# Kernel optimization log

Measured on AMD Instinct MI355X. Metric: run time of the kernel, lower is better.

## Reference

```python
import jax, jax.numpy as jnp
import numpy as np

B, N = 64, 1024
DIMS = [1, 32, 64, 64, 1]   # dim after insert(0,1) and append(1)
DEGS = [2, 2, 2, 2]
EPS = 1e-5


def setup_inputs() -> dict:
    key = jax.random.key(0)
    ks = jax.random.split(key, 16)
    inp = {
        "e": jax.random.uniform(ks[0], (B, N), jnp.float32),
        "phi": jax.random.normal(ks[1], (B, N), jnp.float32),
        "eta": jax.random.normal(ks[2], (B, N), jnp.float32),
    }
    for i in range(4):
        fan_in = DIMS[i] * DEGS[i]
        inp[f"W{i}"] = jax.random.normal(ks[3 + 2 * i], (DIMS[i + 1], fan_in), jnp.float32) / np.sqrt(fan_in)
        inp[f"b{i}"] = jnp.zeros((DIMS[i + 1],), jnp.float32)
    return inp


def _gconv(adj, x, W, b, deg):
    # x: [B, C, N], adj: [B, N, N]
    # operators: [x, x@A, x@A^2, ...] up to deg powers (A^0 = identity)
    ops = [x]
    for _ in range(deg - 1):
        ops.append(jnp.einsum('bcn,bnm->bcm', ops[-1], adj))
    cat = jnp.concatenate(ops, axis=1)                 # [B, C*deg, N]
    return jnp.einsum('oc,bcn->bon', W, cat) + b[None, :, None]


def reference(e, phi, eta, W0, b0, W1, b1, W2, b2, W3, b3):
    # batchnorm(e, axis=1): standardize each event over its particles
    mu = e.mean(axis=1, keepdims=True)
    sd = e.std(axis=1, keepdims=True)
    e = (e - mu) / (sd + EPS)
    e = e[:, None, :]                                   # [B, 1, N]

    # Adjacency: gaussian kernel of squared euclidean distance in (phi, eta)
    d2 = (phi[:, :, None] - phi[:, None, :]) ** 2 + (eta[:, :, None] - eta[:, None, :]) ** 2
    adj = jnp.exp(-d2)                                  # [B, N, N]

    Ws = (W0, W1, W2, W3)
    bs = (b0, b1, b2, b3)
    for i in range(3):
        e = jax.nn.relu(_gconv(adj, e, Ws[i], bs[i], DEGS[i]))
    e = _gconv(adj, e, Ws[3], bs[3], DEGS[3])           # [B, 1, N]

    out = e.mean(axis=2)[:, 0]                          # [B], + logistic_bias (=0)
    return jax.nn.sigmoid(out)
```

## Files before the change

### kernel.cpp

```cpp
#include <hip/hip_runtime.h>
#include <hip/hip_bf16.h>
#include <math.h>

#define BB 64
#define NN 1024
#define EPSV 1e-5f

typedef unsigned short u16;
typedef __attribute__((ext_vector_type(8))) short short8;
typedef __attribute__((ext_vector_type(4))) float f32x4;

#define GLOBAL_AS __attribute__((address_space(1)))
#define LDS_AS __attribute__((address_space(3)))

#define SCL 1.20112240878645f

static __device__ __forceinline__ void gload_lds16(const void* g, void* l) {
  __builtin_amdgcn_global_load_lds((const GLOBAL_AS unsigned int*)g,
                                   (LDS_AS unsigned int*)l, 16, 0, 0);
}

static __device__ __forceinline__ u16 f2bf(float f) {
  __hip_bfloat16 h = __float2bfloat16(f);
  union { __hip_bfloat16 h; u16 s; } u; u.h = h; return u.s;
}
static __device__ __forceinline__ float bf2f(u16 s) {
  unsigned int u = ((unsigned int)s) << 16;
  union { unsigned int u; float f; } c; c.u = u; return c.f;
}
static __device__ __forceinline__ float expn2(float dp, float de) {
#if __has_builtin(__builtin_amdgcn_exp2f)
  return __builtin_amdgcn_exp2f(fmaf(-dp, dp, -(de * de)));
#else
  return exp2f(fmaf(-dp, dp, -(de * de)));
#endif
}

__global__ __launch_bounds__(256, 4) void fused0_kernel(
    const float* __restrict__ e,
    const float* __restrict__ phi, const float* __restrict__ eta,
    const float* __restrict__ W0, const float* __restrict__ b0,
    const float* __restrict__ W1, const float* __restrict__ W2,
    u16* __restrict__ Wp1, u16* __restrict__ Wp2,
    u16* __restrict__ ZN,
    u16* __restrict__ ZC)
{
  __shared__ float x0[NN];
  __shared__ float2 pe[NN];
  __shared__ float red[256];
  __shared__ u16 zt[64 * 40];

  int b = blockIdx.y;
  int m0 = blockIdx.x * 64;
  int tid = threadIdx.x;

  if (blockIdx.x == 0 && b == 0)
    for (int i = tid; i < 64 * 64; i += 256) Wp1[i] = f2bf(W1[i]);
  if (blockIdx.x == 0 && b == 1)
    for (int i = tid; i < 64 * 128; i += 256) Wp2[i] = f2bf(W2[i]);

  const float* er = e + (size_t)b * NN;
  const float* phb = phi + (size_t)b * NN;
  const float* etb = eta + (size_t)b * NN;

  float s = 0.f;
  for (int i = tid; i < NN; i += 256) {
    float v = er[i]; x0[i] = v; s += v;
    pe[i] = make_float2(phb[i] * SCL, etb[i] * SCL);
  }
  red[tid] = s; __syncthreads();
  for (int off = 128; off > 0; off >>= 1) {
    if (tid < off) red[tid] += red[tid + off];
    __syncthreads();
  }
  float mu = red[0] * (1.f / NN);
  __syncthreads();
  float s2 = 0.f;
  for (int i = tid; i < NN; i += 256) { float d = x0[i] - mu; s2 += d * d; }
  red[tid] = s2; __syncthreads();
  for (int off = 128; off > 0; off >>= 1) {
    if (tid < off) red[tid] += red[tid + off];
    __syncthreads();
  }
  float sd = sqrtf(red[0] * (1.f / NN));
  float inv = 1.f / (sd + EPSV);
  for (int i = tid; i < NN; i += 256) x0[i] = (x0[i] - mu) * inv;
  __syncthreads();

  int q = tid >> 6;
  int mi = tid & 63;
  int m = m0 + mi;
  float phm = pe[m].x, etm = pe[m].y;

  const float2* pp = &pe[q * 256];
  const float* xx = &x0[q * 256];
  float t0a = 0.f, t0b = 0.f;
#pragma unroll 4
  for (int n = 0; n < 256; n += 2) {
    float2 qa = pp[n], qb = pp[n + 1];
    float dpa = qa.x - phm, dea = qa.y - etm;
    float dpb = qb.x - phm, deb = qb.y - etm;
    t0a = fmaf(expn2(dpa, dea), xx[n], t0a);
    t0b = fmaf(expn2(dpb, deb), xx[n + 1], t0b);
  }
  red[q * 64 + mi] = t0a + t0b;
  __syncthreads();
  float t0 = (red[0 * 64 + mi] + red[1 * 64 + mi]) +
             (red[2 * 64 + mi] + red[3 * 64 + mi]);

  float x0m = x0[m];
  union { short8 v; u16 h[8]; } zrow;
#pragma unroll
  for (int oj = 0; oj < 8; ++oj) {
    int o = q * 8 + oj;
    float z = fmaf(W0[o * 2], x0m, fmaf(W0[o * 2 + 1], t0, b0[o]));
    zrow.h[oj] = f2bf(fmaxf(z, 0.f));
  }
  *(short8*)&ZN[((size_t)b * NN + m) * 32 + q * 8] = zrow.v;
  *(short8*)&zt[mi * 40 + q * 8] = zrow.v;
  __syncthreads();
  for (int idx = tid; idx < 64 * 32; idx += 256) {
    int mm = idx & 63, o = idx >> 6;
    ZC[((size_t)b * 32 + o) * NN + m0 + mm] = zt[mm * 40 + o];
  }
}

template<int CE, int O, int NT>
__global__ __launch_bounds__(256, 4) void fused_kernel(
    const u16* __restrict__ XC,
    const u16* __restrict__ XN,
    const float* __restrict__ phi,
    const float* __restrict__ eta,
    const u16* __restrict__ Wp,
    const float* __restrict__ bias,
    u16* __restrict__ ZN,
    u16* __restrict__ ZC)
{
  constexpr int NCT = CE / 16;
  constexpr int SLABV = NT * CE / 8;
  constexpr int KW = 2 * CE;
  constexpr int S = KW + 8;
  constexpr int OT = O / 16;
  constexpr int KS = KW / 32;
  constexpr int STEPS = NN / NT;
  constexpr int KCN = NT / 32;

  constexpr int PH1 = (int)sizeof(float2) * NN + 2 * NT * CE * 2;
  constexpr int PH2 = 64 * S * 2;
  constexpr int ZTS = 64 * (O + 8) * 2;
  constexpr int SM0 = PH1 > PH2 ? PH1 : PH2;
  constexpr int SM = SM0 > ZTS ? SM0 : ZTS;
  __shared__ __align__(16) char smem[SM];
  float2* pe = (float2*)smem;
  u16* slab0 = (u16*)(smem + sizeof(float2) * NN);
  u16* slab1 = slab0 + NT * CE;
  u16* cat = (u16*)smem;
  u16* zt  = (u16*)smem;

  int b = blockIdx.y;
  int m0 = blockIdx.x * 64;
  int tid = threadIdx.x;
  int lane = tid & 63, w = tid >> 6, g = lane >> 4, cl = lane & 15;

  const float* phb = phi + (size_t)b * NN;
  const float* etb = eta + (size_t)b * NN;
  for (int i = tid; i < NN; i += 256)
    pe[i] = make_float2(phb[i] * SCL, etb[i] * SCL);

  int m_lane = m0 + w * 16 + cl;
  float phm = phb[m_lane] * SCL;
  float etm = etb[m_lane] * SCL;

  f32x4 acc[NCT];
#pragma unroll
  for (int ci = 0; ci < NCT; ++ci) acc[ci] = (f32x4){0.f, 0.f, 0.f, 0.f};

  const u16* xb = XC + (size_t)b * CE * NN;

  for (int v = tid; v < SLABV; v += 256) {
    int gg = v / CE, cc = (v % CE) ^ (gg & 7);
    gload_lds16(xb + (size_t)cc * NN + gg * 8, slab0 + v * 8);
  }
  __syncthreads();

  for (int s = 0; s < STEPS; ++s) {
    u16* curp = (s & 1) ? slab1 : slab0;
    u16* nxtp = (s & 1) ? slab0 : slab1;
    if (s + 1 < STEPS) {
      for (int v = tid; v < SLABV; v += 256) {
        int gg = v / CE, cc = (v % CE) ^ (gg & 7);
        gload_lds16(xb + (size_t)cc * NN + (s + 1) * NT + gg * 8, nxtp + v * 8);
      }
    }
    int n0 = s * NT;
#pragma unroll
    for (int kc = 0; kc < KCN; ++kc) {
      const float2* pp = &pe[n0 + kc * 32 + 8 * g];
      union { short8 v; u16 h[8]; } af;
#pragma unroll
      for (int j = 0; j < 8; ++j) {
        float2 qq = pp[j];
        af.h[j] = f2bf(expn2(qq.x - phm, qq.y - etm));
      }
      int ggr = kc * 4 + g, sw = ggr & 7;
#pragma unroll
      for (int ci = 0; ci < NCT; ++ci) {
        const short8* bp =
            (const short8*)&curp[(ggr * CE + ((ci * 16 + cl) ^ sw)) * 8];
        acc[ci] = __builtin_amdgcn_mfma_f32_16x16x32_bf16(af.v, *bp, acc[ci], 0, 0, 0);
      }
    }
    __syncthreads();
  }

  constexpr int CV = CE / 8;
  constexpr int NXN = (64 * CV + 255) / 256;
  constexpr bool XFULL = (64 * CV) % 256 == 0;
  short8 xnr[NXN];
#pragma unroll
  for (int i = 0; i < NXN; ++i) {
    int v = tid + i * 256;
    if (XFULL || v < 64 * CV) {
      int m = v / CV, cv = v % CV;
      xnr[i] = *(const short8*)&XN[((size_t)b * NN + m0 + m) * CE + cv * 8];
    }
  }
  float bz[OT];
#pragma unroll
  for (int oi = 0; oi < OT; ++oi) bz[oi] = bias[oi * 16 + cl];

#pragma unroll
  for (int ci = 0; ci < NCT; ++ci)
#pragma unroll
    for (int r = 0; r < 4; ++r) {
      int m = w * 16 + g * 4 + r;
      cat[m * S + CE + ci * 16 + cl] = f2bf(acc[ci][r]);
    }
#pragma unroll
  for (int i = 0; i < NXN; ++i) {
    int v = tid + i * 256;
    if (XFULL || v < 64 * CV) {
      int m = v / CV, cv = v % CV;
      *(short8*)&cat[m * S + cv * 8] = xnr[i];
    }
  }
  __syncthreads();

  short8 afp[KS];
#pragma unroll
  for (int kk = 0; kk < KS; ++kk)
    afp[kk] = *(const short8*)&cat[(w * 16 + cl) * S + kk * 32 + g * 8];

  constexpr int OB = (8 / KS) < OT ? (8 / KS) : OT;
  f32x4 pacc[OT];
#pragma unroll
  for (int oi = 0; oi < OT; ++oi) pacc[oi] = (f32x4){0.f, 0.f, 0.f, 0.f};
#pragma unroll
  for (int ob = 0; ob < OT; ob += OB) {
    short8 wfr[OB][KS];
#pragma unroll
    for (int oi = 0; oi < OB; ++oi)
#pragma unroll
      for (int kk = 0; kk < KS; ++kk)
        wfr[oi][kk] = *(const short8*)&Wp[((ob + oi) * 16 + cl) * KW + kk * 32 + g * 8];
#pragma unroll
    for (int oi = 0; oi < OB; ++oi)
#pragma unroll
      for (int kk = 0; kk < KS; ++kk)
        pacc[ob + oi] = __builtin_amdgcn_mfma_f32_16x16x32_bf16(
            afp[kk], wfr[oi][kk], pacc[ob + oi], 0, 0, 0);
  }
  __syncthreads();

#pragma unroll
  for (int oi = 0; oi < OT; ++oi) {
#pragma unroll
    for (int r = 0; r < 4; ++r) {
      float z = fmaxf(pacc[oi][r] + bz[oi], 0.f);
      u16 zb = f2bf(z);
      int m = w * 16 + 4 * g + r;
      ZN[((size_t)b * NN + m0 + m) * O + oi * 16 + cl] = zb;
      zt[m * (O + 8) + oi * 16 + cl] = zb;
    }
  }
  __syncthreads();
  for (int idx = tid; idx < 64 * O; idx += 256) {
    int m = idx & 63, o = idx >> 6;
    ZC[((size_t)b * O + o) * NN + m0 + m] = zt[m * (O + 8) + o];
  }
}

__global__ __launch_bounds__(256, 4) void fused_last_kernel(
    const u16* __restrict__ XC,
    const u16* __restrict__ XN,
    const float* __restrict__ phi,
    const float* __restrict__ eta,
    const float* __restrict__ W3,
    const float* __restrict__ b3,
    float* __restrict__ partial)
{
  constexpr int CE = 64, NCT = 4, NT = 128;
  constexpr int SLABV = NT * CE / 8;
  constexpr int S = 136;
  constexpr int STEPS = NN / NT;

  constexpr int PH1 = (int)sizeof(float2) * NN + 2 * NT * CE * 2;
  __shared__ __align__(16) char smem[PH1];
  float2* pe = (float2*)smem;
  u16* slab0 = (u16*)(smem + sizeof(float2) * NN);
  u16* slab1 = slab0 + NT * CE;
  u16* cat = (u16*)smem;
  float* sW = (float*)(smem + 17408);
  float* red = (float*)(smem + 17408 + 512);

  int b = blockIdx.y;
  int m0 = blockIdx.x * 64;
  int tid = threadIdx.x;
  int lane = tid & 63, w = tid >> 6, g = lane >> 4, cl = lane & 15;

  const float* phb = phi + (size_t)b * NN;
  const float* etb = eta + (size_t)b * NN;
  for (int i = tid; i < NN; i += 256)
    pe[i] = make_float2(phb[i] * SCL, etb[i] * SCL);

  int m_lane = m0 + w * 16 + cl;
  float phm = phb[m_lane] * SCL;
  float etm = etb[m_lane] * SCL;

  f32x4 acc[NCT];
#pragma unroll
  for (int ci = 0; ci < NCT; ++ci) acc[ci] = (f32x4){0.f, 0.f, 0.f, 0.f};

  const u16* xb = XC + (size_t)b * CE * NN;

  for (int v = tid; v < SLABV; v += 256) {
    int gg = v / CE, cc = (v % CE) ^ (gg & 7);
    gload_lds16(xb + (size_t)cc * NN + gg * 8, slab0 + v * 8);
  }
  __syncthreads();

  for (int s = 0; s < STEPS; ++s) {
    u16* curp = (s & 1) ? slab1 : slab0;
    u16* nxtp = (s & 1) ? slab0 : slab1;
    if (s + 1 < STEPS) {
      for (int v = tid; v < SLABV; v += 256) {
        int gg = v / CE, cc = (v % CE) ^ (gg & 7);
        gload_lds16(xb + (size_t)cc * NN + (s + 1) * NT + gg * 8, nxtp + v * 8);
      }
    }
    int n0 = s * NT;
#pragma unroll
    for (int kc = 0; kc < NT / 32; ++kc) {
      const float2* pp = &pe[n0 + kc * 32 + 8 * g];
      union { short8 v; u16 h[8]; } af;
#pragma unroll
      for (int j = 0; j < 8; ++j) {
        float2 qq = pp[j];
        af.h[j] = f2bf(expn2(qq.x - phm, qq.y - etm));
      }
      int ggr = kc * 4 + g, sw = ggr & 7;
#pragma unroll
      for (int ci = 0; ci < NCT; ++ci) {
        const short8* bp =
            (const short8*)&curp[(ggr * CE + ((ci * 16 + cl) ^ sw)) * 8];
        acc[ci] = __builtin_amdgcn_mfma_f32_16x16x32_bf16(af.v, *bp, acc[ci], 0, 0, 0);
      }
    }
    __syncthreads();
  }

  short8 xnr0, xnr1;
  {
    int v0 = tid, v1 = tid + 256;
    int ma = v0 >> 3, ca = v0 & 7, mb = v1 >> 3, cb = v1 & 7;
    xnr0 = *(const short8*)&XN[((size_t)b * NN + m0 + ma) * CE + ca * 8];
    xnr1 = *(const short8*)&XN[((size_t)b * NN + m0 + mb) * CE + cb * 8];
  }
  if (tid < 128) sW[tid] = W3[tid];
#pragma unroll
  for (int ci = 0; ci < NCT; ++ci)
#pragma unroll
    for (int r = 0; r < 4; ++r) {
      int m = w * 16 + g * 4 + r;
      cat[m * S + CE + ci * 16 + cl] = f2bf(acc[ci][r]);
    }
  {
    int v0 = tid, v1 = tid + 256;
    int ma = v0 >> 3, ca = v0 & 7, mb = v1 >> 3, cb = v1 & 7;
    *(short8*)&cat[ma * S + ca * 8] = xnr0;
    *(short8*)&cat[mb * S + cb * 8] = xnr1;
  }
  __syncthreads();

  int m = tid & 63, q = tid >> 6;
  float sacc = 0.f;
#pragma unroll
  for (int v = 0; v < 4; ++v) {
    short8 cv = *(const short8*)&cat[m * S + q * 32 + v * 8];
#pragma unroll
    for (int j = 0; j < 8; ++j)
      sacc = fmaf(sW[q * 32 + v * 8 + j], bf2f((u16)cv[j]), sacc);
  }
  red[tid] = sacc; __syncthreads();
  for (int off = 128; off > 0; off >>= 1) {
    if (tid < off) red[tid] += red[tid + off];
    __syncthreads();
  }
  if (tid == 0)
    partial[b * 16 + blockIdx.x] = red[0] + 64.f * b3[0];
}

__global__ __launch_bounds__(64) void final_kernel(const float* __restrict__ partial,
                                                   float* __restrict__ out) {
  int b = blockIdx.x;
  int lane = threadIdx.x;
  float v = (lane < 16) ? partial[b * 16 + lane] : 0.f;
#pragma unroll
  for (int off = 8; off > 0; off >>= 1) v += __shfl_down(v, off);
  if (lane == 0) out[b] = 1.f / (1.f + __expf(-(v * (1.f / NN))));
}

extern "C" void kernel_launch(void* const* d_in, const int* in_sizes, int n_in,
                              void* d_out, int out_size, void* d_ws, size_t ws_size,
                              hipStream_t stream) {
  const float* e   = (const float*)d_in[0];
  const float* phi = (const float*)d_in[1];
  const float* eta = (const float*)d_in[2];
  const float* W0  = (const float*)d_in[3];
  const float* b0  = (const float*)d_in[4];
  const float* W1  = (const float*)d_in[5];
  const float* b1  = (const float*)d_in[6];
  const float* W2  = (const float*)d_in[7];
  const float* b2  = (const float*)d_in[8];
  const float* W3  = (const float*)d_in[9];
  const float* b3  = (const float*)d_in[10];

  char* wsb = (char*)d_ws;
  const size_t MB = 1u << 20;
  float* PB = (float*)(wsb);
  u16* XC1 = (u16*)(wsb + 12 * MB);
  u16* XN1 = (u16*)(wsb + 16 * MB);
  u16* XC2 = (u16*)(wsb + 20 * MB);
  u16* XN2 = (u16*)(wsb + 28 * MB);
  u16* XC3 = (u16*)(wsb + 8 * MB);
  u16* XN3 = (u16*)(wsb + 36 * MB);
  u16* Wp1 = (u16*)(wsb + 44 * MB);
  u16* Wp2 = Wp1 + 64 * 64;

  dim3 blk(256);
  dim3 gg(NN / 64, BB);

  fused0_kernel<<<gg, blk, 0, stream>>>(e, phi, eta, W0, b0, W1, W2,
                                        Wp1, Wp2, XN1, XC1);
  fused_kernel<32, 64, 128><<<gg, blk, 0, stream>>>(XC1, XN1, phi, eta, Wp1, b1, XN2, XC2);
  fused_kernel<64, 64, 128><<<gg, blk, 0, stream>>>(XC2, XN2, phi, eta, Wp2, b2, XN3, XC3);
  fused_last_kernel<<<gg, blk, 0, stream>>>(XC3, XN3, phi, eta, W3, b3, PB);

  final_kernel<<<BB, dim3(64), 0, stream>>>(PB, (float*)d_out);
}
```

Measured before the change: 113.1 us.

## Use blocked channel-interleaved activation layout and triple-buffered LDS pipeline

Activations for the next layer are now written in a blocked layout of 8 consecutive nodes times all channels, so each staged slab is one contiguous chunk of global memory instead of CE strided rows. The x@A loop now uses 64-node steps with a three-slot LDS ring, prefetches two steps ahead, and waits with explicit vmcnt counts plus a single raw barrier per step instead of two full syncthreads. The aim is more coalesced loads and more load/compute overlap. In exchange there are twice as many steps and a hand-written waitcnt sequence that depends on the exact count of outstanding loads.

```diff
diff --git a/kernel.cpp b/kernel.cpp
--- a/kernel.cpp
+++ b/kernel.cpp
@@ -34,6 +34,14 @@
 #else
   return exp2f(fmaf(-dp, dp, -(de * de)));
 #endif
+}
+
+template<int N>
+static __device__ __forceinline__ void wait_vm() {
+  static_assert(N == 0 || N == 1 || N == 2, "");
+  if constexpr (N == 0) asm volatile("s_waitcnt vmcnt(0)" ::: "memory");
+  if constexpr (N == 1) asm volatile("s_waitcnt vmcnt(1)" ::: "memory");
+  if constexpr (N == 2) asm volatile("s_waitcnt vmcnt(2)" ::: "memory");
 }
 
 __global__ __launch_bounds__(256, 4) void fused0_kernel(
@@ -43,7 +51,7 @@
     const float* __restrict__ W1, const float* __restrict__ W2,
     u16* __restrict__ Wp1, u16* __restrict__ Wp2,
     u16* __restrict__ ZN,
-    u16* __restrict__ ZC)
+    u16* __restrict__ XT)
 {
   __shared__ float x0[NN];
   __shared__ float2 pe[NN];
@@ -119,25 +127,31 @@
   *(short8*)&ZN[((size_t)b * NN + m) * 32 + q * 8] = zrow.v;
   *(short8*)&zt[mi * 40 + q * 8] = zrow.v;
   __syncthreads();
-  for (int idx = tid; idx < 64 * 32; idx += 256) {
-    int mm = idx & 63, o = idx >> 6;
-    ZC[((size_t)b * 32 + o) * NN + m0 + mm] = zt[mm * 40 + o];
-  }
-}
-
-template<int CE, int O, int NT>
+  size_t basew = ((size_t)b * (NN / 8) + (m0 >> 3)) * (size_t)(32 * 8);
+  for (int flat = tid; flat < 64 * 32; flat += 256) {
+    int mo = flat >> 8;
+    int o  = (flat >> 3) & 31;
+    int m8 = flat & 7;
+    XT[basew + flat] = zt[(mo * 8 + m8) * 40 + o];
+  }
+}
+
+template<int CE, int O>
 __global__ __launch_bounds__(256, 4) void fused_kernel(
-    const u16* __restrict__ XC,
+    const u16* __restrict__ XT,
     const u16* __restrict__ XN,
     const float* __restrict__ phi,
     const float* __restrict__ eta,
     const u16* __restrict__ Wp,
     const float* __restrict__ bias,
     u16* __restrict__ ZN,
-    u16* __restrict__ ZC)
+    u16* __restrict__ XTo)
 {
+  constexpr int NT = 64;
   constexpr int NCT = CE / 16;
-  constexpr int SLABV = NT * CE / 8;
+  constexpr int SLAB = NT * CE;
+  constexpr int SLABV = SLAB / 8;
+  constexpr int LPT = SLABV / 256;
   constexpr int KW = 2 * CE;
   constexpr int S = KW + 8;
   constexpr int OT = O / 16;
@@ -145,15 +159,14 @@
   constexpr int STEPS = NN / NT;
   constexpr int KCN = NT / 32;
 
-  constexpr int PH1 = (int)sizeof(float2) * NN + 2 * NT * CE * 2;
+  constexpr int PH1 = (int)sizeof(float2) * NN + 3 * SLAB * 2;
   constexpr int PH2 = 64 * S * 2;
   constexpr int ZTS = 64 * (O + 8) * 2;
   constexpr int SM0 = PH1 > PH2 ? PH1 : PH2;
   constexpr int SM = SM0 > ZTS ? SM0 : ZTS;
   __shared__ __align__(16) char smem[SM];
   float2* pe = (float2*)smem;
-  u16* slab0 = (u16*)(smem + sizeof(float2) * NN);
-  u16* slab1 = slab0 + NT * CE;
+  u16* slabB = (u16*)(smem + sizeof(float2) * NN);
   u16* cat = (u16*)smem;
   u16* zt  = (u16*)smem;
 
@@ -175,23 +188,31 @@
 #pragma unroll
   for (int ci = 0; ci < NCT; ++ci) acc[ci] = (f32x4){0.f, 0.f, 0.f, 0.f};
 
-  const u16* xb = XC + (size_t)b * CE * NN;
-
-  for (int v = tid; v < SLABV; v += 256) {
-    int gg = v / CE, cc = (v % CE) ^ (gg & 7);
-    gload_lds16(xb + (size_t)cc * NN + gg * 8, slab0 + v * 8);
-  }
-  __syncthreads();
+  const u16* xtb = XT + (size_t)b * NN * CE;
+
+  auto stage = [&](int step, u16* dst) {
+#pragma unroll
+    for (int k = 0; k < LPT; ++k) {
+      int v = tid + k * 256;
+      int gg = v / CE, cc = v % CE;
+      int cs = cc ^ (gg & 7);
+      gload_lds16(xtb + ((size_t)((step * NT >> 3) + gg) * CE + cs) * 8,
+                  dst + v * 8);
+    }
+  };
+
+  __syncthreads();
+  stage(0, slabB);
+  stage(1, slabB + SLAB);
 
   for (int s = 0; s < STEPS; ++s) {
-    u16* curp = (s & 1) ? slab1 : slab0;
-    u16* nxtp = (s & 1) ? slab0 : slab1;
-    if (s + 1 < STEPS) {
-      for (int v = tid; v < SLABV; v += 256) {
-        int gg = v / CE, cc = (v % CE) ^ (gg & 7);
-        gload_lds16(xb + (size_t)cc * NN + (s + 1) * NT + gg * 8, nxtp + v * 8);
-      }
-    }
+    __builtin_amdgcn_sched_barrier(0);
+    if (s + 1 < STEPS) wait_vm<LPT>(); else wait_vm<0>();
+    __builtin_amdgcn_s_barrier();
+    __builtin_amdgcn_sched_barrier(0);
+    if (s + 2 < STEPS) stage(s + 2, slabB + ((s + 2) % 3) * SLAB);
+
+    const u16* cur = slabB + (s % 3) * SLAB;
     int n0 = s * NT;
 #pragma unroll
     for (int kc = 0; kc < KCN; ++kc) {
@@ -206,12 +227,12 @@
 #pragma unroll
       for (int ci = 0; ci < NCT; ++ci) {
         const short8* bp =
-            (const short8*)&curp[(ggr * CE + ((ci * 16 + cl) ^ sw)) * 8];
+            (const short8*)&cur[(ggr * CE + ((ci * 16 + cl) ^ sw)) * 8];
         acc[ci] = __builtin_amdgcn_mfma_f32_16x16x32_bf16(af.v, *bp, acc[ci], 0, 0, 0);
       }
     }
-    __syncthreads();
-  }
+  }
+  __syncthreads();
 
   constexpr int CV = CE / 8;
   constexpr int NXN = (64 * CV + 255) / 256;
@@ -284,14 +305,17 @@
     }
   }
   __syncthreads();
-  for (int idx = tid; idx < 64 * O; idx += 256) {
-    int m = idx & 63, o = idx >> 6;
-    ZC[((size_t)b * O + o) * NN + m0 + m] = zt[m * (O + 8) + o];
+  size_t basew = ((size_t)b * (NN / 8) + (m0 >> 3)) * (size_t)(O * 8);
+  for (int flat = tid; flat < 64 * O; flat += 256) {
+    int mo = flat / (O * 8);
+    int o  = (flat >> 3) % O;
+    int m8 = flat & 7;
+    XTo[basew + flat] = zt[(mo * 8 + m8) * (O + 8) + o];
   }
 }
 
 __global__ __launch_bounds__(256, 4) void fused_last_kernel(
-    const u16* __restrict__ XC,
+    const u16* __restrict__ XT,
     const u16* __restrict__ XN,
     const float* __restrict__ phi,
     const float* __restrict__ eta,
@@ -299,16 +323,18 @@
     const float* __restrict__ b3,
     float* __restrict__ partial)
 {
-  constexpr int CE = 64, NCT = 4, NT = 128;
-  constexpr int SLABV = NT * CE / 8;
+  constexpr int CE = 64, NCT = 4, NT = 64;
+  constexpr int SLAB = NT * CE;
+  constexpr int SLABV = SLAB / 8;
+  constexpr int LPT = SLABV / 256;
   constexpr int S = 136;
   constexpr int STEPS = NN / NT;
-
-  constexpr int PH1 = (int)sizeof(float2) * NN + 2 * NT * CE * 2;
+  constexpr int KCN = NT / 32;
+
+  constexpr int PH1 = (int)sizeof(float2) * NN + 3 * SLAB * 2;
   __shared__ __align__(16) char smem[PH1];
   float2* pe = (float2*)smem;
-  u16* slab0 = (u16*)(smem + sizeof(float2) * NN);
-  u16* slab1 = slab0 + NT * CE;
+  u16* slabB = (u16*)(smem + sizeof(float2) * NN);
   u16* cat = (u16*)smem;
   float* sW = (float*)(smem + 17408);
   float* red = (float*)(smem + 17408 + 512);
@@ -331,26 +357,34 @@
 #pragma unroll
   for (int ci = 0; ci < NCT; ++ci) acc[ci] = (f32x4){0.f, 0.f, 0.f, 0.f};
 
-  const u16* xb = XC + (size_t)b * CE * NN;
-
-  for (int v = tid; v < SLABV; v += 256) {
-    int gg = v / CE, cc = (v % CE) ^ (gg & 7);
-    gload_lds16(xb + (size_t)cc * NN + gg * 8, slab0 + v * 8);
-  }
-  __syncthreads();
+  const u16* xtb = XT + (size_t)b * NN * CE;
+
+  auto stage = [&](int step, u16* dst) {
+#pragma unroll
+    for (int k = 0; k < LPT; ++k) {
+      int v = tid + k * 256;
+      int gg = v / CE, cc = v % CE;
+      int cs = cc ^ (gg & 7);
+      gload_lds16(xtb + ((size_t)((step * NT >> 3) + gg) * CE + cs) * 8,
+                  dst + v * 8);
+    }
+  };
+
+  __syncthreads();
+  stage(0, slabB);
+  stage(1, slabB + SLAB);
 
   for (int s = 0; s < STEPS; ++s) {
-    u16* curp = (s & 1) ? slab1 : slab0;
-    u16* nxtp = (s & 1) ? slab0 : slab1;
-    if (s + 1 < STEPS) {
-      for (int v = tid; v < SLABV; v += 256) {
-        int gg = v / CE, cc = (v % CE) ^ (gg & 7);
-        gload_lds16(xb + (size_t)cc * NN + (s + 1) * NT + gg * 8, nxtp + v * 8);
-      }
-    }
+    __builtin_amdgcn_sched_barrier(0);
+    if (s + 1 < STEPS) wait_vm<LPT>(); else wait_vm<0>();
+    __builtin_amdgcn_s_barrier();
+    __builtin_amdgcn_sched_barrier(0);
+    if (s + 2 < STEPS) stage(s + 2, slabB + ((s + 2) % 3) * SLAB);
+
+    const u16* cur = slabB + (s % 3) * SLAB;
     int n0 = s * NT;
 #pragma unroll
-    for (int kc = 0; kc < NT / 32; ++kc) {
+    for (int kc = 0; kc < KCN; ++kc) {
       const float2* pp = &pe[n0 + kc * 32 + 8 * g];
       union { short8 v; u16 h[8]; } af;
 #pragma unroll
@@ -362,12 +396,12 @@
 #pragma unroll
       for (int ci = 0; ci < NCT; ++ci) {
         const short8* bp =
-            (const short8*)&curp[(ggr * CE + ((ci * 16 + cl) ^ sw)) * 8];
+            (const short8*)&cur[(ggr * CE + ((ci * 16 + cl) ^ sw)) * 8];
         acc[ci] = __builtin_amdgcn_mfma_f32_16x16x32_bf16(af.v, *bp, acc[ci], 0, 0, 0);
       }
     }
-    __syncthreads();
-  }
+  }
+  __syncthreads();
 
   short8 xnr0, xnr1;
   {
@@ -438,11 +472,11 @@
   char* wsb = (char*)d_ws;
   const size_t MB = 1u << 20;
   float* PB = (float*)(wsb);
-  u16* XC1 = (u16*)(wsb + 12 * MB);
-  u16* XN1 = (u16*)(wsb + 16 * MB);
-  u16* XC2 = (u16*)(wsb + 20 * MB);
-  u16* XN2 = (u16*)(wsb + 28 * MB);
-  u16* XC3 = (u16*)(wsb + 8 * MB);
+  u16* XT1 = (u16*)(wsb + 4 * MB);
+  u16* XN1 = (u16*)(wsb + 8 * MB);
+  u16* XT2 = (u16*)(wsb + 12 * MB);
+  u16* XN2 = (u16*)(wsb + 20 * MB);
+  u16* XT3 = (u16*)(wsb + 28 * MB);
   u16* XN3 = (u16*)(wsb + 36 * MB);
   u16* Wp1 = (u16*)(wsb + 44 * MB);
   u16* Wp2 = Wp1 + 64 * 64;
@@ -451,10 +485,10 @@
   dim3 gg(NN / 64, BB);
 
   fused0_kernel<<<gg, blk, 0, stream>>>(e, phi, eta, W0, b0, W1, W2,
-                                        Wp1, Wp2, XN1, XC1);
-  fused_kernel<32, 64, 128><<<gg, blk, 0, stream>>>(XC1, XN1, phi, eta, Wp1, b1, XN2, XC2);
-  fused_kernel<64, 64, 128><<<gg, blk, 0, stream>>>(XC2, XN2, phi, eta, Wp2, b2, XN3, XC3);
-  fused_last_kernel<<<gg, blk, 0, stream>>>(XC3, XN3, phi, eta, W3, b3, PB);
+                                        Wp1, Wp2, XN1, XT1);
+  fused_kernel<32, 64><<<gg, blk, 0, stream>>>(XT1, XN1, phi, eta, Wp1, b1, XN2, XT2);
+  fused_kernel<64, 64><<<gg, blk, 0, stream>>>(XT2, XN2, phi, eta, Wp2, b2, XN3, XT3);
+  fused_last_kernel<<<gg, blk, 0, stream>>>(XT3, XN3, phi, eta, W3, b3, PB);
 
   final_kernel<<<BB, dim3(64), 0, stream>>>(PB, (float*)d_out);
 }
```

Result: faster. 103.8 us (-8.2%).
